# Kernel optimization log

Measured on AMD Instinct MI355X. Metric: run time of the kernel, lower is better.

Reference implementation:

```python
import jax, jax.numpy as jnp
import numpy as np

B, Q, HID = 16, 1, 1024
LH, LD = 32, 128            # large num heads / large head dim
BLOCK, NBPS = 16, 64        # cache block size, blocks per sequence
NBLK, MAXLEN = B * NBPS, NBPS * BLOCK
ROPE_BASE = 10000.0


def setup_inputs() -> dict:
    key = jax.random.key(0)
    ks = jax.random.split(key, 6)
    hidden_states = jax.random.normal(ks[0], (B, Q, HID), jnp.float32)
    q_proj_w = jax.random.normal(ks[1], (LH * LD, HID), jnp.float32) * 0.02
    o_proj_w = jax.random.normal(ks[2], (HID, LH * LD), jnp.float32) * 0.02
    k_cache = jax.random.normal(ks[3], (NBLK, LH, BLOCK, LD), jnp.float32)
    v_cache = jax.random.normal(ks[4], (NBLK, LH, BLOCK, LD), jnp.float32)
    # each sequence owns NBPS distinct cache blocks
    block_tables = jnp.arange(NBLK, dtype=jnp.int32).reshape(B, NBPS)
    sequence_lengths = jax.random.randint(ks[5], (B,), 1, MAXLEN + 1).astype(jnp.int32)
    position_ids = (sequence_lengths - 1).astype(jnp.int32).reshape(B, Q)
    return dict(hidden_states=hidden_states, q_proj_w=q_proj_w, o_proj_w=o_proj_w,
                k_cache=k_cache, v_cache=v_cache, block_tables=block_tables,
                sequence_lengths=sequence_lengths, position_ids=position_ids,
                n_spec_tokens=5)


def _rotate_half(x):
    h = x.shape[-1] // 2
    return jnp.concatenate([-x[..., h:], x[..., :h]], axis=-1)


def reference(hidden_states, q_proj_w, o_proj_w, k_cache, v_cache,
              block_tables, sequence_lengths, position_ids, n_spec_tokens):
    # q projection -> [B, Q, LH, LD]
    q = (hidden_states @ q_proj_w.T).reshape(B, Q, LH, LD)
    # RoPE at positions shifted by n_spec_tokens
    pos = (position_ids + n_spec_tokens).astype(jnp.float32)              # [B, Q]
    inv_freq = 1.0 / (ROPE_BASE ** (jnp.arange(0, LD, 2, dtype=jnp.float32) / LD))
    freqs = pos[..., None] * inv_freq                                      # [B, Q, LD/2]
    emb = jnp.concatenate([freqs, freqs], axis=-1)                         # [B, Q, LD]
    cos = jnp.cos(emb)[:, :, None, :]
    sin = jnp.sin(emb)[:, :, None, :]
    q = q * cos + _rotate_half(q) * sin
    q = q.reshape(B * Q, LH, LD)  # q_len == 1 -> [B, LH, LD]
    # gather paged KV: [B, NBPS, LH, BLOCK, LD] -> [B, L, LH, LD]
    k = k_cache[block_tables].transpose(0, 1, 3, 2, 4).reshape(B, MAXLEN, LH, LD)
    v = v_cache[block_tables].transpose(0, 1, 3, 2, 4).reshape(B, MAXLEN, LH, LD)
    scale = float(1.0 / np.sqrt(LD))
    scores = jnp.einsum('bhd,blhd->bhl', q, k) * scale                     # [B, LH, L]
    valid = jnp.arange(MAXLEN)[None, :] < sequence_lengths[:, None]        # [B, L]
    scores = jnp.where(valid[:, None, :], scores, -jnp.inf)
    attn = jax.nn.softmax(scores, axis=-1)
    out = jnp.einsum('bhl,blhd->bhd', attn, v).reshape(B, Q, LH * LD)
    return out @ o_proj_w.T                                                # [B, Q, HID]
```

## Files before the change

kernel.cpp:

```cpp
#include <hip/hip_runtime.h>
#include <hip/hip_bf16.h>
#include <math.h>

#define B_   16
#define HID_ 1024
#define LH_  32
#define LD_  128
#define BLOCK_ 16
#define NBPS_  64
#define MAXLEN_ 1024
#define SPLIT_ 16
#define CHUNK_ (MAXLEN_ / SPLIT_)

typedef float vf4 __attribute__((ext_vector_type(4)));

__global__ __launch_bounds__(256) void qproj_rope_kernel(const float* __restrict__ hs,
                                                         const float* __restrict__ w,
                                                         const int* __restrict__ pid,
                                                         const int* __restrict__ nsp,
                                                         float* __restrict__ q) {
    int t = threadIdx.x;
    int h = blockIdx.x >> 3;
    int g = blockIdx.x & 7;
    __shared__ float shs[16 * 1024];
    __shared__ float ssum[16][16];
    {
        const vf4* src = (const vf4*)hs;
        vf4* dst = (vf4*)shs;
        for (int i = t; i < 4096; i += 256) dst[i] = src[i];
    }
    int j  = t >> 5;
    int sl = t & 31;
    int r0 = h * 128 + g * 8 + j;
    int r1 = r0 + 64;
    vf4 w0[8], w1[8];
#pragma unroll
    for (int s = 0; s < 8; ++s) {
        w0[s] = *(const vf4*)&w[(size_t)r0 * HID_ + s * 128 + sl * 4];
        w1[s] = *(const vf4*)&w[(size_t)r1 * HID_ + s * 128 + sl * 4];
    }
    __syncthreads();
    for (int b = 0; b < B_; ++b) {
        float p0 = 0.f, p1 = 0.f;
#pragma unroll
        for (int s = 0; s < 8; ++s) {
            vf4 a = *(const vf4*)&shs[b * 1024 + s * 128 + sl * 4];
            p0 += w0[s].x*a.x + w0[s].y*a.y + w0[s].z*a.z + w0[s].w*a.w;
            p1 += w1[s].x*a.x + w1[s].y*a.y + w1[s].z*a.z + w1[s].w*a.w;
        }
#pragma unroll
        for (int o = 1; o < 32; o <<= 1) { p0 += __shfl_xor(p0, o); p1 += __shfl_xor(p1, o); }
        if (sl == 0) { ssum[j][b] = p0; ssum[j + 8][b] = p1; }
    }
    __syncthreads();
    if (t < 128) {
        int jj = t >> 4;
        int b  = t & 15;
        int d  = g * 8 + jj;
        double x0 = (double)ssum[jj][b];
        double x1 = (double)ssum[jj + 8][b];
        double pos = (double)(pid[b] + nsp[0]);
        double inv_freq = 1.0 / pow(10000.0, (double)d * (1.0 / 64.0));
        double f = pos * inv_freq;
        double cs = cos(f), sn = sin(f);
        const double scale = 0.08838834764831845;
        int base = b * 4096 + h * LD_ + d;
        q[base]      = (float)((x0 * cs - x1 * sn) * scale);
        q[base + 64] = (float)((x1 * cs + x0 * sn) * scale);
    }
}

__global__ __launch_bounds__(256) void attn_kernel(const float* __restrict__ q,
                                                   const float* __restrict__ kc,
                                                   const float* __restrict__ vc,
                                                   const int* __restrict__ btab,
                                                   const int* __restrict__ slen,
                                                   float* __restrict__ pml,
                                                   float* __restrict__ pacc) {
    int c = blockIdx.x, h = blockIdx.y, b = blockIdx.z;
    int L = slen[b];
    int start = c * CHUNK_;
    int bh = b * LH_ + h;
    int pbase = bh * SPLIT_ + c;
    int t = threadIdx.x;

    if (start >= L) {
        if (t < 128) pacc[(size_t)pbase * 128 + t] = 0.f;
        if (t == 0) { pml[pbase * 2] = -INFINITY; pml[pbase * 2 + 1] = 0.f; }
        return;
    }

    int lane = t & 63, wv = t >> 6;
    int sg = lane >> 4;
    int lg = lane & 15;
    int d0 = lg * 8;
    int po = wv * 4 + sg;
    const float* qp = q + (size_t)bh * LD_ + d0;
    vf4 qa = *(const vf4*)qp;
    vf4 qb = *(const vf4*)(qp + 4);

    int end = min(start + CHUNK_, L);
    int blkr[4];
#pragma unroll
    for (int i = 0; i < 4; ++i) blkr[i] = btab[b * NBPS_ + c * 4 + i];

    float m = -INFINITY, l = 0.f;
    float acc[8];
#pragma unroll
    for (int k = 0; k < 8; ++k) acc[k] = 0.f;

    int i = 0;
#pragma unroll 4
    for (int pos = start + po; pos < end; pos += 16, ++i) {
        size_t off = (((size_t)blkr[i] * LH_ + h) * BLOCK_ + po) * LD_ + d0;
        vf4 k0 = *(const vf4*)(kc + off);
        vf4 k1 = *(const vf4*)(kc + off + 4);
        vf4 v0 = *(const vf4*)(vc + off);
        vf4 v1 = *(const vf4*)(vc + off + 4);

        float dot = qa.x*k0.x + qa.y*k0.y + qa.z*k0.z + qa.w*k0.w
                  + qb.x*k1.x + qb.y*k1.y + qb.z*k1.z + qb.w*k1.w;
#pragma unroll
        for (int o = 1; o < 16; o <<= 1) dot += __shfl_xor(dot, o);

        float mn = fmaxf(m, dot);
        float r = (m >= mn) ? 1.f : __expf(m - mn);
        float p = __expf(dot - mn);
        l = l * r + p;
        acc[0] = acc[0]*r + p*v0.x;  acc[1] = acc[1]*r + p*v0.y;
        acc[2] = acc[2]*r + p*v0.z;  acc[3] = acc[3]*r + p*v0.w;
        acc[4] = acc[4]*r + p*v1.x;  acc[5] = acc[5]*r + p*v1.y;
        acc[6] = acc[6]*r + p*v1.z;  acc[7] = acc[7]*r + p*v1.w;
        m = mn;
    }

#pragma unroll
    for (int o = 16; o < 64; o <<= 1) {
        float m2 = __shfl_xor(m, o), l2 = __shfl_xor(l, o);
        float a2[8];
#pragma unroll
        for (int k = 0; k < 8; ++k) a2[k] = __shfl_xor(acc[k], o);
        float mn = fmaxf(m, m2);
        float ra = (m  >= mn) ? 1.f : __expf(m  - mn);
        float rb = (m2 >= mn) ? 1.f : __expf(m2 - mn);
        l = l * ra + l2 * rb;
#pragma unroll
        for (int k = 0; k < 8; ++k) acc[k] = acc[k]*ra + a2[k]*rb;
        m = mn;
    }

    __shared__ float sm[4], sl_[4], sacc[4][128];
    if (lane < 16) {
#pragma unroll
        for (int k = 0; k < 8; ++k) sacc[wv][d0 + k] = acc[k];
        if (lane == 0) { sm[wv] = m; sl_[wv] = l; }
    }
    __syncthreads();

    if (t < 64) {
        float M = fmaxf(fmaxf(sm[0], sm[1]), fmaxf(sm[2], sm[3]));
        int d = t * 2;
        float lt = 0.f, o0 = 0.f, o1 = 0.f;
#pragma unroll
        for (int w2 = 0; w2 < 4; ++w2) {
            float mw = sm[w2];
            float e = (mw >= M) ? 1.f : __expf(mw - M);
            lt += e * sl_[w2];
            o0 += e * sacc[w2][d];
            o1 += e * sacc[w2][d + 1];
        }
        pacc[(size_t)pbase * 128 + d]     = o0;
        pacc[(size_t)pbase * 128 + d + 1] = o1;
        if (t == 0) { pml[pbase * 2] = M; pml[pbase * 2 + 1] = lt; }
    }
}

__global__ __launch_bounds__(64) void combine_kernel(const float* __restrict__ pml,
                                                     const float* __restrict__ pacc,
                                                     float* __restrict__ attn) {
    int bh = blockIdx.x;
    int lane = threadIdx.x;
    float M = -INFINITY;
#pragma unroll
    for (int c = 0; c < SPLIT_; ++c) M = fmaxf(M, pml[(bh * SPLIT_ + c) * 2]);
    int d = lane * 2;
    float lt = 0.f, o0 = 0.f, o1 = 0.f;
#pragma unroll
    for (int c = 0; c < SPLIT_; ++c) {
        float mc = pml[(bh * SPLIT_ + c) * 2];
        float e = (mc >= M) ? 1.f : __expf(mc - M);
        lt += e * pml[(bh * SPLIT_ + c) * 2 + 1];
        o0 += e * pacc[((size_t)bh * SPLIT_ + c) * 128 + d];
        o1 += e * pacc[((size_t)bh * SPLIT_ + c) * 128 + d + 1];
    }
    float inv = 1.f / lt;
    attn[(size_t)bh * LD_ + d]     = o0 * inv;
    attn[(size_t)bh * LD_ + d + 1] = o1 * inv;
}

__global__ __launch_bounds__(256) void oproj_kernel(const float* __restrict__ attn,
                                                    const float* __restrict__ w,
                                                    float* __restrict__ out) {
    int t = threadIdx.x;
    int row0 = blockIdx.x * 4;
    float wr[4][16];
#pragma unroll
    for (int r = 0; r < 4; ++r)
#pragma unroll
        for (int s = 0; s < 16; ++s)
            wr[r][s] = w[(size_t)(row0 + r) * 4096 + t + 256 * s];

    int lane = t & 63, wv = t >> 6;
    __shared__ float lds[16][4][4];
    for (int b = 0; b < B_; ++b) {
        float p[4] = {0.f, 0.f, 0.f, 0.f};
#pragma unroll
        for (int s = 0; s < 16; ++s) {
            float a = attn[b * 4096 + t + 256 * s];
#pragma unroll
            for (int r = 0; r < 4; ++r) p[r] += wr[r][s] * a;
        }
#pragma unroll
        for (int off = 32; off; off >>= 1)
#pragma unroll
            for (int r = 0; r < 4; ++r) p[r] += __shfl_xor(p[r], off);
        if (lane == 0)
#pragma unroll
            for (int r = 0; r < 4; ++r) lds[b][wv][r] = p[r];
    }
    __syncthreads();
    if (t < 64) {
        int b = t >> 2, r = t & 3;
        out[b * HID_ + row0 + r] = lds[b][0][r] + lds[b][1][r] + lds[b][2][r] + lds[b][3][r];
    }
}

extern "C" void kernel_launch(void* const* d_in, const int* in_sizes, int n_in,
                              void* d_out, int out_size, void* d_ws, size_t ws_size,
                              hipStream_t stream) {
    const float* hs   = (const float*)d_in[0];
    const float* qw   = (const float*)d_in[1];
    const float* ow   = (const float*)d_in[2];
    const float* kc   = (const float*)d_in[3];
    const float* vc   = (const float*)d_in[4];
    const int*   btab = (const int*)d_in[5];
    const int*   slen = (const int*)d_in[6];
    const int*   pid  = (const int*)d_in[7];
    const int*   nsp  = (const int*)d_in[8];
    float* out = (float*)d_out;
    float* ws  = (float*)d_ws;

    float* q_ws    = ws;
    float* attn_ws = ws + 65536;
    float* pml     = ws + 131072;
    float* pacc    = ws + 147456;

    qproj_rope_kernel<<<256, 256, 0, stream>>>(hs, qw, pid, nsp, q_ws);
    attn_kernel<<<dim3(SPLIT_, LH_, B_), 256, 0, stream>>>(q_ws, kc, vc, btab, slen, pml, pacc);
    combine_kernel<<<B_ * LH_, 64, 0, stream>>>(pml, pacc, attn_ws);
    oproj_kernel<<<256, 256, 0, stream>>>(attn_ws, ow, out);
}
```

Baseline: 109.6 us.

## Map each attention split chunk to one wavefront and drop LDS staging

The attention kernel now gives each 64-lane wavefront its own (batch, head, chunk) item, with each 16-lane subgroup walking one contiguous cache block. This removes the per-block LDS reduction and `__syncthreads`, and the waves store their partial max, sum and accumulator directly. Chunks past the sequence length write nothing, and the combine kernel reads only the valid chunks based on the sequence length. The q projection also reads hidden states straight from global memory (via cache) instead of staging 64KB in LDS. The trade-off is a longer sequential loop per wave and fewer waves in flight, which may reduce memory-level parallelism.

```diff
diff --git a/kernel.cpp b/kernel.cpp
--- a/kernel.cpp
+++ b/kernel.cpp
@@ -22,13 +22,7 @@
     int t = threadIdx.x;
     int h = blockIdx.x >> 3;
     int g = blockIdx.x & 7;
-    __shared__ float shs[16 * 1024];
     __shared__ float ssum[16][16];
-    {
-        const vf4* src = (const vf4*)hs;
-        vf4* dst = (vf4*)shs;
-        for (int i = t; i < 4096; i += 256) dst[i] = src[i];
-    }
     int j  = t >> 5;
     int sl = t & 31;
     int r0 = h * 128 + g * 8 + j;
@@ -39,12 +33,11 @@
         w0[s] = *(const vf4*)&w[(size_t)r0 * HID_ + s * 128 + sl * 4];
         w1[s] = *(const vf4*)&w[(size_t)r1 * HID_ + s * 128 + sl * 4];
     }
-    __syncthreads();
     for (int b = 0; b < B_; ++b) {
         float p0 = 0.f, p1 = 0.f;
 #pragma unroll
         for (int s = 0; s < 8; ++s) {
-            vf4 a = *(const vf4*)&shs[b * 1024 + s * 128 + sl * 4];
+            vf4 a = *(const vf4*)&hs[b * 1024 + s * 128 + sl * 4];
             p0 += w0[s].x*a.x + w0[s].y*a.y + w0[s].z*a.z + w0[s].w*a.w;
             p1 += w1[s].x*a.x + w1[s].y*a.y + w1[s].z*a.z + w1[s].w*a.w;
         }
@@ -77,42 +70,39 @@
                                                    const int* __restrict__ slen,
                                                    float* __restrict__ pml,
                                                    float* __restrict__ pacc) {
-    int c = blockIdx.x, h = blockIdx.y, b = blockIdx.z;
+    int t = threadIdx.x;
+    int wv = t >> 6, lane = t & 63;
+    int item = blockIdx.x * 4 + wv;
+    int c = item & (SPLIT_ - 1);
+    int h = (item >> 4) & (LH_ - 1);
+    int b = item >> 9;
     int L = slen[b];
     int start = c * CHUNK_;
-    int bh = b * LH_ + h;
-    int pbase = bh * SPLIT_ + c;
-    int t = threadIdx.x;
-
-    if (start >= L) {
-        if (t < 128) pacc[(size_t)pbase * 128 + t] = 0.f;
-        if (t == 0) { pml[pbase * 2] = -INFINITY; pml[pbase * 2 + 1] = 0.f; }
-        return;
-    }
-
-    int lane = t & 63, wv = t >> 6;
+    if (start >= L) return;
+
     int sg = lane >> 4;
     int lg = lane & 15;
     int d0 = lg * 8;
-    int po = wv * 4 + sg;
+    int bh = b * LH_ + h;
+    int pbase = bh * SPLIT_ + c;
+
     const float* qp = q + (size_t)bh * LD_ + d0;
     vf4 qa = *(const vf4*)qp;
     vf4 qb = *(const vf4*)(qp + 4);
 
-    int end = min(start + CHUNK_, L);
-    int blkr[4];
-#pragma unroll
-    for (int i = 0; i < 4; ++i) blkr[i] = btab[b * NBPS_ + c * 4 + i];
+    int blk = btab[b * NBPS_ + c * 4 + sg];
+    int nv = L - start - sg * 16;
+    nv = nv < 0 ? 0 : (nv > 16 ? 16 : nv);
+    size_t off0 = (((size_t)blk * LH_ + h) * BLOCK_) * LD_ + d0;
 
     float m = -INFINITY, l = 0.f;
     float acc[8];
 #pragma unroll
     for (int k = 0; k < 8; ++k) acc[k] = 0.f;
 
-    int i = 0;
 #pragma unroll 4
-    for (int pos = start + po; pos < end; pos += 16, ++i) {
-        size_t off = (((size_t)blkr[i] * LH_ + h) * BLOCK_ + po) * LD_ + d0;
+    for (int i = 0; i < nv; ++i) {
+        size_t off = off0 + (size_t)i * LD_;
         vf4 k0 = *(const vf4*)(kc + off);
         vf4 k1 = *(const vf4*)(kc + off + 4);
         vf4 v0 = *(const vf4*)(vc + off);
@@ -149,44 +139,29 @@
         m = mn;
     }
 
-    __shared__ float sm[4], sl_[4], sacc[4][128];
     if (lane < 16) {
-#pragma unroll
-        for (int k = 0; k < 8; ++k) sacc[wv][d0 + k] = acc[k];
-        if (lane == 0) { sm[wv] = m; sl_[wv] = l; }
-    }
-    __syncthreads();
-
-    if (t < 64) {
-        float M = fmaxf(fmaxf(sm[0], sm[1]), fmaxf(sm[2], sm[3]));
-        int d = t * 2;
-        float lt = 0.f, o0 = 0.f, o1 = 0.f;
-#pragma unroll
-        for (int w2 = 0; w2 < 4; ++w2) {
-            float mw = sm[w2];
-            float e = (mw >= M) ? 1.f : __expf(mw - M);
-            lt += e * sl_[w2];
-            o0 += e * sacc[w2][d];
-            o1 += e * sacc[w2][d + 1];
-        }
-        pacc[(size_t)pbase * 128 + d]     = o0;
-        pacc[(size_t)pbase * 128 + d + 1] = o1;
-        if (t == 0) { pml[pbase * 2] = M; pml[pbase * 2 + 1] = lt; }
+        float* pd = pacc + (size_t)pbase * 128 + d0;
+        vf4 s0 = {acc[0], acc[1], acc[2], acc[3]};
+        vf4 s1 = {acc[4], acc[5], acc[6], acc[7]};
+        *(vf4*)pd = s0;
+        *(vf4*)(pd + 4) = s1;
+        if (lane == 0) { pml[pbase * 2] = m; pml[pbase * 2 + 1] = l; }
     }
 }
 
 __global__ __launch_bounds__(64) void combine_kernel(const float* __restrict__ pml,
                                                      const float* __restrict__ pacc,
+                                                     const int* __restrict__ slen,
                                                      float* __restrict__ attn) {
     int bh = blockIdx.x;
+    int b = bh >> 5;
+    int cmax = (slen[b] + CHUNK_ - 1) >> 6;
     int lane = threadIdx.x;
     float M = -INFINITY;
-#pragma unroll
-    for (int c = 0; c < SPLIT_; ++c) M = fmaxf(M, pml[(bh * SPLIT_ + c) * 2]);
+    for (int c = 0; c < cmax; ++c) M = fmaxf(M, pml[(bh * SPLIT_ + c) * 2]);
     int d = lane * 2;
     float lt = 0.f, o0 = 0.f, o1 = 0.f;
-#pragma unroll
-    for (int c = 0; c < SPLIT_; ++c) {
+    for (int c = 0; c < cmax; ++c) {
         float mc = pml[(bh * SPLIT_ + c) * 2];
         float e = (mc >= M) ? 1.f : __expf(mc - M);
         lt += e * pml[(bh * SPLIT_ + c) * 2 + 1];
@@ -256,7 +231,7 @@
     float* pacc    = ws + 147456;
 
     qproj_rope_kernel<<<256, 256, 0, stream>>>(hs, qw, pid, nsp, q_ws);
-    attn_kernel<<<dim3(SPLIT_, LH_, B_), 256, 0, stream>>>(q_ws, kc, vc, btab, slen, pml, pacc);
-    combine_kernel<<<B_ * LH_, 64, 0, stream>>>(pml, pacc, attn_ws);
+    attn_kernel<<<2048, 256, 0, stream>>>(q_ws, kc, vc, btab, slen, pml, pacc);
+    combine_kernel<<<B_ * LH_, 64, 0, stream>>>(pml, pacc, slen, attn_ws);
     oproj_kernel<<<256, 256, 0, stream>>>(attn_ws, ow, out);
 }
```

Measured after the change: 123.3 us. 12.5% more time.

## Double grid for projections, drop LDS staging, skip dead attention chunks in combine

Applied to the files above, without the earlier changes.

The q-projection kernel now uses 512 blocks with 4 rows per wave-pair instead of 8. It reads hidden states directly from global memory instead of staging 64KB into LDS, so the large shared footprint no longer limits occupancy. The o-projection also moves to 512 blocks with 2 rows each and vectorized float4 weight loads. Attention blocks past the sequence length now exit without writing partials, and combine loops only over valid chunks derived from the sequence length. The trade-off is redundant global reads of hidden states and attention rows across more blocks.

```diff
diff --git a/kernel.cpp b/kernel.cpp
--- a/kernel.cpp
+++ b/kernel.cpp
@@ -20,51 +20,47 @@
                                                          const int* __restrict__ nsp,
                                                          float* __restrict__ q) {
     int t = threadIdx.x;
-    int h = blockIdx.x >> 3;
-    int g = blockIdx.x & 7;
-    __shared__ float shs[16 * 1024];
-    __shared__ float ssum[16][16];
-    {
-        const vf4* src = (const vf4*)hs;
-        vf4* dst = (vf4*)shs;
-        for (int i = t; i < 4096; i += 256) dst[i] = src[i];
-    }
-    int j  = t >> 5;
-    int sl = t & 31;
-    int r0 = h * 128 + g * 8 + j;
+    int h = blockIdx.x >> 4;
+    int g = blockIdx.x & 15;
+    int j = t >> 6;
+    int lane = t & 63;
+    int d = g * 4 + j;
+    int r0 = h * 128 + d;
     int r1 = r0 + 64;
-    vf4 w0[8], w1[8];
-#pragma unroll
-    for (int s = 0; s < 8; ++s) {
-        w0[s] = *(const vf4*)&w[(size_t)r0 * HID_ + s * 128 + sl * 4];
-        w1[s] = *(const vf4*)&w[(size_t)r1 * HID_ + s * 128 + sl * 4];
-    }
-    __syncthreads();
+
+    vf4 w0[4], w1[4];
+#pragma unroll
+    for (int s = 0; s < 4; ++s) {
+        w0[s] = *(const vf4*)&w[(size_t)r0 * HID_ + s * 256 + lane * 4];
+        w1[s] = *(const vf4*)&w[(size_t)r1 * HID_ + s * 256 + lane * 4];
+    }
+
+    __shared__ float ssum[8][16];
     for (int b = 0; b < B_; ++b) {
         float p0 = 0.f, p1 = 0.f;
 #pragma unroll
-        for (int s = 0; s < 8; ++s) {
-            vf4 a = *(const vf4*)&shs[b * 1024 + s * 128 + sl * 4];
+        for (int s = 0; s < 4; ++s) {
+            vf4 a = *(const vf4*)&hs[b * 1024 + s * 256 + lane * 4];
             p0 += w0[s].x*a.x + w0[s].y*a.y + w0[s].z*a.z + w0[s].w*a.w;
             p1 += w1[s].x*a.x + w1[s].y*a.y + w1[s].z*a.z + w1[s].w*a.w;
         }
 #pragma unroll
-        for (int o = 1; o < 32; o <<= 1) { p0 += __shfl_xor(p0, o); p1 += __shfl_xor(p1, o); }
-        if (sl == 0) { ssum[j][b] = p0; ssum[j + 8][b] = p1; }
+        for (int o = 1; o < 64; o <<= 1) { p0 += __shfl_xor(p0, o); p1 += __shfl_xor(p1, o); }
+        if (lane == 0) { ssum[j][b] = p0; ssum[j + 4][b] = p1; }
     }
     __syncthreads();
-    if (t < 128) {
+    if (t < 64) {
         int jj = t >> 4;
         int b  = t & 15;
-        int d  = g * 8 + jj;
+        int dd = g * 4 + jj;
         double x0 = (double)ssum[jj][b];
-        double x1 = (double)ssum[jj + 8][b];
+        double x1 = (double)ssum[jj + 4][b];
         double pos = (double)(pid[b] + nsp[0]);
-        double inv_freq = 1.0 / pow(10000.0, (double)d * (1.0 / 64.0));
+        double inv_freq = 1.0 / pow(10000.0, (double)dd * (1.0 / 64.0));
         double f = pos * inv_freq;
         double cs = cos(f), sn = sin(f);
         const double scale = 0.08838834764831845;
-        int base = b * 4096 + h * LD_ + d;
+        int base = b * 4096 + h * LD_ + dd;
         q[base]      = (float)((x0 * cs - x1 * sn) * scale);
         q[base + 64] = (float)((x1 * cs + x0 * sn) * scale);
     }
@@ -80,16 +76,11 @@
     int c = blockIdx.x, h = blockIdx.y, b = blockIdx.z;
     int L = slen[b];
     int start = c * CHUNK_;
+    if (start >= L) return;
+
     int bh = b * LH_ + h;
     int pbase = bh * SPLIT_ + c;
     int t = threadIdx.x;
-
-    if (start >= L) {
-        if (t < 128) pacc[(size_t)pbase * 128 + t] = 0.f;
-        if (t == 0) { pml[pbase * 2] = -INFINITY; pml[pbase * 2 + 1] = 0.f; }
-        return;
-    }
-
     int lane = t & 63, wv = t >> 6;
     int sg = lane >> 4;
     int lg = lane & 15;
@@ -177,16 +168,17 @@
 
 __global__ __launch_bounds__(64) void combine_kernel(const float* __restrict__ pml,
                                                      const float* __restrict__ pacc,
+                                                     const int* __restrict__ slen,
                                                      float* __restrict__ attn) {
     int bh = blockIdx.x;
+    int b = bh >> 5;
+    int cmax = (slen[b] + CHUNK_ - 1) >> 6;
     int lane = threadIdx.x;
     float M = -INFINITY;
-#pragma unroll
-    for (int c = 0; c < SPLIT_; ++c) M = fmaxf(M, pml[(bh * SPLIT_ + c) * 2]);
+    for (int c = 0; c < cmax; ++c) M = fmaxf(M, pml[(bh * SPLIT_ + c) * 2]);
     int d = lane * 2;
     float lt = 0.f, o0 = 0.f, o1 = 0.f;
-#pragma unroll
-    for (int c = 0; c < SPLIT_; ++c) {
+    for (int c = 0; c < cmax; ++c) {
         float mc = pml[(bh * SPLIT_ + c) * 2];
         float e = (mc >= M) ? 1.f : __expf(mc - M);
         lt += e * pml[(bh * SPLIT_ + c) * 2 + 1];
@@ -202,36 +194,34 @@
                                                     const float* __restrict__ w,
                                                     float* __restrict__ out) {
     int t = threadIdx.x;
-    int row0 = blockIdx.x * 4;
-    float wr[4][16];
-#pragma unroll
-    for (int r = 0; r < 4; ++r)
-#pragma unroll
-        for (int s = 0; s < 16; ++s)
-            wr[r][s] = w[(size_t)(row0 + r) * 4096 + t + 256 * s];
-
+    int row0 = blockIdx.x * 2;
     int lane = t & 63, wv = t >> 6;
-    __shared__ float lds[16][4][4];
+
+    vf4 wr0[4], wr1[4];
+#pragma unroll
+    for (int s = 0; s < 4; ++s) {
+        wr0[s] = *(const vf4*)&w[(size_t)row0 * 4096 + s * 1024 + t * 4];
+        wr1[s] = *(const vf4*)&w[(size_t)(row0 + 1) * 4096 + s * 1024 + t * 4];
+    }
+
+    __shared__ float lds[2][4][16];
     for (int b = 0; b < B_; ++b) {
-        float p[4] = {0.f, 0.f, 0.f, 0.f};
-#pragma unroll
-        for (int s = 0; s < 16; ++s) {
-            float a = attn[b * 4096 + t + 256 * s];
-#pragma unroll
-            for (int r = 0; r < 4; ++r) p[r] += wr[r][s] * a;
+        float p0 = 0.f, p1 = 0.f;
+#pragma unroll
+        for (int s = 0; s < 4; ++s) {
+            vf4 a = *(const vf4*)&attn[b * 4096 + s * 1024 + t * 4];
+            p0 += wr0[s].x*a.x + wr0[s].y*a.y + wr0[s].z*a.z + wr0[s].w*a.w;
+            p1 += wr1[s].x*a.x + wr1[s].y*a.y + wr1[s].z*a.z + wr1[s].w*a.w;
         }
 #pragma unroll
-        for (int off = 32; off; off >>= 1)
-#pragma unroll
-            for (int r = 0; r < 4; ++r) p[r] += __shfl_xor(p[r], off);
-        if (lane == 0)
-#pragma unroll
-            for (int r = 0; r < 4; ++r) lds[b][wv][r] = p[r];
+        for (int o = 1; o < 64; o <<= 1) { p0 += __shfl_xor(p0, o); p1 += __shfl_xor(p1, o); }
+        if (lane == 0) { lds[0][wv][b] = p0; lds[1][wv][b] = p1; }
     }
     __syncthreads();
-    if (t < 64) {
-        int b = t >> 2, r = t & 3;
-        out[b * HID_ + row0 + r] = lds[b][0][r] + lds[b][1][r] + lds[b][2][r] + lds[b][3][r];
+    if (t < 32) {
+        int r = t >> 4, b = t & 15;
+        out[b * HID_ + row0 + r] =
+            lds[r][0][b] + lds[r][1][b] + lds[r][2][b] + lds[r][3][b];
     }
 }
 
@@ -255,8 +245,8 @@
     float* pml     = ws + 131072;
     float* pacc    = ws + 147456;
 
-    qproj_rope_kernel<<<256, 256, 0, stream>>>(hs, qw, pid, nsp, q_ws);
+    qproj_rope_kernel<<<512, 256, 0, stream>>>(hs, qw, pid, nsp, q_ws);
     attn_kernel<<<dim3(SPLIT_, LH_, B_), 256, 0, stream>>>(q_ws, kc, vc, btab, slen, pml, pacc);
-    combine_kernel<<<B_ * LH_, 64, 0, stream>>>(pml, pacc, attn_ws);
-    oproj_kernel<<<256, 256, 0, stream>>>(attn_ws, ow, out);
-}
+    combine_kernel<<<B_ * LH_, 64, 0, stream>>>(pml, pacc, slen, attn_ws);
+    oproj_kernel<<<512, 256, 0, stream>>>(attn_ws, ow, out);
+}
```

New measurement: 110.4 us. About the same (+0.7%).
